# Kernel optimization log

Hardware: AMD Instinct MI355X
Metric: run time of the kernel (lower is better)

## Reference

```python
import jax, jax.numpy as jnp
import numpy as np

B, L = 8, 2048
AMP, ANG = 48, 16
H = 4
AQK, GQK = 12, 6   # amp/ang qk head dims
AV, GV = 12, 6     # amp/ang v head dims
LOOKBACK = 100


def setup_inputs() -> dict:
    key = jax.random.key(0)
    ks = jax.random.split(key, 16)
    def w(k, i, o):
        # kaiming-uniform-ish scale; stored [in, out] so forward is x @ W
        bound = 1.0 / np.sqrt(i)
        return jax.random.uniform(k, (i, o), jnp.float32, -bound, bound)
    return dict(
        x_ang=jax.random.normal(ks[0], (B, L, 2 * ANG), jnp.float32),
        x_amp=jax.random.normal(ks[1], (B, L, AMP), jnp.float32),
        Wq_amp=w(ks[2], AMP, H * AQK),
        Wk_amp=w(ks[3], AMP, H * AQK),
        Wv_amp=w(ks[4], AMP, H * AV),
        Wq_ang_r=w(ks[5], ANG, H * GQK),
        Wq_ang_i=w(ks[6], ANG, H * GQK),
        Wk_ang_r=w(ks[7], ANG, H * GQK),
        Wk_ang_i=w(ks[8], ANG, H * GQK),
        Wv_ang_r=w(ks[9], ANG, H * GV),
        Wv_ang_i=w(ks[10], ANG, H * GV),
        Wout_amp=w(ks[11], H * AV, AMP),
        bout_amp=jax.random.uniform(ks[12], (AMP,), jnp.float32, -0.1, 0.1),
        Wout_ang_r=w(ks[13], H * GV, ANG),
        Wout_ang_i=w(ks[14], H * GV, ANG),
    )


def _clin(xr, xi, Wr, Wi):
    # complex linear: (xr + i xi) @ (Wr + i Wi)
    return xr @ Wr - xi @ Wi, xr @ Wi + xi @ Wr


def reference(x_ang, x_amp, Wq_amp, Wk_amp, Wv_amp,
              Wq_ang_r, Wq_ang_i, Wk_ang_r, Wk_ang_i,
              Wv_ang_r, Wv_ang_i, Wout_amp, bout_amp,
              Wout_ang_r, Wout_ang_i):
    Bb, Ll, CA = x_ang.shape
    ang_r, ang_i = jnp.split(x_ang, 2, axis=-1)

    def heads(x, hd):  # [B,L,H*hd] -> [B,H,L,hd]
        return x.reshape(Bb, Ll, H, hd).transpose(0, 2, 1, 3)

    q_amp = heads(x_amp @ Wq_amp, AQK)
    k_amp = heads(x_amp @ Wk_amp, AQK)
    qar, qai = _clin(ang_r, ang_i, Wq_ang_r, Wq_ang_i)
    kar, kai = _clin(ang_r, ang_i, Wk_ang_r, Wk_ang_i)
    q = jnp.concatenate([heads(qar, GQK), heads(qai, GQK), q_amp], axis=-1)  # [B,H,L,24]
    k = jnp.concatenate([heads(kar, GQK), heads(kai, GQK), k_amp], axis=-1)

    v_amp = heads(x_amp @ Wv_amp, AV)
    var, vai = _clin(ang_r, ang_i, Wv_ang_r, Wv_ang_i)
    v = jnp.concatenate([heads(var, GV), heads(vai, GV), v_amp], axis=-1)  # [B,H,L,24]

    scale = 1.0 / jnp.sqrt(jnp.asarray(q.shape[-1], q.dtype))
    scores = jnp.einsum('bhqd,bhkd->bhqk', q, k) * scale
    idx = jnp.arange(Ll)
    valid = (idx[None, :] <= idx[:, None]) & (idx[None, :] >= idx[:, None] - (LOOKBACK - 1))
    mask = jnp.where(valid, jnp.asarray(0.0, scores.dtype), jnp.finfo(scores.dtype).min)
    attn = jax.nn.softmax(scores + mask, axis=-1)
    out = jnp.einsum('bhqk,bhkd->bhqd', attn, v)  # [B,H,L,24]

    o_ang_r, o_ang_i, o_amp = jnp.split(out, [GV, 2 * GV], axis=-1)

    def merge(x):  # [B,H,L,hd] -> [B,L,H*hd]
        return x.transpose(0, 2, 1, 3).reshape(Bb, Ll, -1)

    out_amp = merge(o_amp) @ Wout_amp + bout_amp
    out_ang_r, out_ang_i = _clin(merge(o_ang_r), merge(o_ang_i), Wout_ang_r, Wout_ang_i)
    return (out_ang_r, out_ang_i, out_amp)
```

## Files before the change

kernel.cpp:

```cpp
#include <hip/hip_runtime.h>
#include <hip/hip_bf16.h>

constexpr int B = 8;
constexpr int L = 2048;
constexpr int ANG = 16;
constexpr int AMP = 48;
constexpr int H = 4;
constexpr int AQK = 12, GQK = 6;
constexpr int AV = 12, GV = 6;
constexpr int HD = 2 * GQK + AQK;
constexpr int LOOKBACK = 100;
constexpr int NTOK = B * L;

constexpr int TQ     = 64;
constexpr int GROUPS = 4;
constexpr int MAXK   = TQ + LOOKBACK - 1;
constexpr int NT     = L / TQ;

struct StageT {
    float xam[MAXK][49];
    float xan[MAXK][33];
};
struct TileT {
    float4 Ks[MAXK][8];
    float4 Vs[MAXK][8];
    float4 Qs[TQ][6];
};
union SharedU { StageT stage; TileT t; };

__global__ __launch_bounds__(256) void fused_qkv_attn_kernel(
    const float* __restrict__ x_ang, const float* __restrict__ x_amp,
    const float* __restrict__ Wq_amp, const float* __restrict__ Wk_amp,
    const float* __restrict__ Wv_amp,
    const float* __restrict__ Wq_ang_r, const float* __restrict__ Wq_ang_i,
    const float* __restrict__ Wk_ang_r, const float* __restrict__ Wk_ang_i,
    const float* __restrict__ Wv_ang_r, const float* __restrict__ Wv_ang_i,
    float* __restrict__ att)
{
    __shared__ SharedU u;
    __shared__ float  Pm[GROUPS][TQ];
    __shared__ float  Ps[GROUPS][TQ];
    __shared__ float4 Po[GROUPS][TQ][6];

    const int tid = threadIdx.x;
    const int bh  = blockIdx.x / NT;
    const int qt  = blockIdx.x % NT;
    const int b   = bh / H, h = bh % H;
    const int q0  = qt * TQ;
    int kmin = q0 - (LOOKBACK - 1); if (kmin < 0) kmin = 0;
    const int nrows = (q0 + TQ - 1) - kmin + 1;
    const int qoff  = q0 - kmin;

    {
        const float4* xm4 = (const float4*)(x_amp + ((size_t)b * L + kmin) * AMP);
        const float4* xg4 = (const float4*)(x_ang + ((size_t)b * L + kmin) * (2 * ANG));
        int namp = nrows * 12;
        int ntot = namp + nrows * 8;
        for (int c = tid; c < ntot; c += 256) {
            if (c < namp) {
                int r = c / 12, i = c % 12;
                float4 t = xm4[c];
                float* p = &u.stage.xam[r][4 * i];
                p[0] = t.x; p[1] = t.y; p[2] = t.z; p[3] = t.w;
            } else {
                int c2 = c - namp;
                int r = c2 / 8, i = c2 % 8;
                float4 t = xg4[c2];
                float* p = &u.stage.xan[r][4 * i];
                p[0] = t.x; p[1] = t.y; p[2] = t.z; p[3] = t.w;
            }
        }
    }
    __syncthreads();

    float4 kout[6], vout[6], qout[6];
    const bool kvact = (tid < nrows);
    const bool qact  = (tid >= 192);
    const int  qrow  = tid - 192;

    #pragma unroll
    for (int s = 0; s < 6; ++s) {
        if (kvact) {
            int r = tid;
            if (s >= 3) {
                int col4 = h * AQK + (s - 3) * 4;
                const float* Wk = Wk_amp + col4;
                const float* Wv = Wv_amp + col4;
                float4 ka = {0,0,0,0}, va = {0,0,0,0};
                #pragma unroll
                for (int i = 0; i < AMP; ++i) {
                    float x = u.stage.xam[r][i];
                    float4 wk = *(const float4*)(Wk + i * 48);
                    float4 wv = *(const float4*)(Wv + i * 48);
                    ka.x += x * wk.x; ka.y += x * wk.y; ka.z += x * wk.z; ka.w += x * wk.w;
                    va.x += x * wv.x; va.y += x * wv.y; va.z += x * wv.z; va.w += x * wv.w;
                }
                kout[s] = ka; vout[s] = va;
            } else {
                float kk[4], vv[4];
                #pragma unroll
                for (int c = 0; c < 4; ++c) {
                    int d = 4 * s + c;
                    bool re = (d < GQK);
                    int dd = re ? d : d - GQK;
                    int col = h * GQK + dd;
                    const float* WkA = re ? Wk_ang_r : Wk_ang_i;
                    const float* WkB = re ? Wk_ang_i : Wk_ang_r;
                    const float* WvA = re ? Wv_ang_r : Wv_ang_i;
                    const float* WvB = re ? Wv_ang_i : Wv_ang_r;
                    float sgn = re ? -1.f : 1.f;
                    float ak = 0, bk = 0, aw = 0, bw = 0;
                    #pragma unroll
                    for (int i = 0; i < ANG; ++i) {
                        float xr = u.stage.xan[r][i];
                        float xi = u.stage.xan[r][16 + i];
                        ak += xr * WkA[i * 24 + col];  bk += xi * WkB[i * 24 + col];
                        aw += xr * WvA[i * 24 + col];  bw += xi * WvB[i * 24 + col];
                    }
                    kk[c] = ak + sgn * bk;  vv[c] = aw + sgn * bw;
                }
                kout[s] = make_float4(kk[0], kk[1], kk[2], kk[3]);
                vout[s] = make_float4(vv[0], vv[1], vv[2], vv[3]);
            }
        }
        if (qact) {
            int r = qoff + qrow;
            if (s >= 3) {
                int col4 = h * AQK + (s - 3) * 4;
                const float* Wq = Wq_amp + col4;
                float4 qa = {0,0,0,0};
                #pragma unroll
                for (int i = 0; i < AMP; ++i) {
                    float x = u.stage.xam[r][i];
                    float4 wq = *(const float4*)(Wq + i * 48);
                    qa.x += x * wq.x; qa.y += x * wq.y; qa.z += x * wq.z; qa.w += x * wq.w;
                }
                qout[s] = qa;
            } else {
                float qq[4];
                #pragma unroll
                for (int c = 0; c < 4; ++c) {
                    int d = 4 * s + c;
                    bool re = (d < GQK);
                    int dd = re ? d : d - GQK;
                    int col = h * GQK + dd;
                    const float* WA = re ? Wq_ang_r : Wq_ang_i;
                    const float* WB = re ? Wq_ang_i : Wq_ang_r;
                    float sgn = re ? -1.f : 1.f;
                    float aa = 0, bb = 0;
                    #pragma unroll
                    for (int i = 0; i < ANG; ++i) {
                        float xr = u.stage.xan[r][i];
                        float xi = u.stage.xan[r][16 + i];
                        aa += xr * WA[i * 24 + col];  bb += xi * WB[i * 24 + col];
                    }
                    qq[c] = aa + sgn * bb;
                }
                qout[s] = make_float4(qq[0], qq[1], qq[2], qq[3]);
            }
        }
    }
    __syncthreads();

    if (kvact) {
        int r = tid, rx = r & 7;
        #pragma unroll
        for (int s = 0; s < 6; ++s) {
            u.t.Ks[r][s ^ rx] = kout[s];
            u.t.Vs[r][s ^ rx] = vout[s];
        }
    }
    if (qact) {
        #pragma unroll
        for (int s = 0; s < 6; ++s) u.t.Qs[qrow][s] = qout[s];
    }
    __syncthreads();

    const int qlocal = tid & (TQ - 1);
    const int group  = tid >> 6;
    const int qi = q0 + qlocal;

    float4 qr4[6];
    #pragma unroll
    for (int s = 0; s < 6; ++s) qr4[s] = u.t.Qs[qlocal][s];

    const float scale = 0.2041241452319315f;
    float m = -3.0e38f, ss = 0.f;
    float4 o4[6];
    #pragma unroll
    for (int s = 0; s < 6; ++s) { o4[s].x = 0.f; o4[s].y = 0.f; o4[s].z = 0.f; o4[s].w = 0.f; }

    int j0 = qi - (LOOKBACK - 1); if (j0 < 0) j0 = 0;
    for (int j = j0 + group; j <= qi; j += GROUPS) {
        int r  = j - kmin;
        int rx = r & 7;
        float sc = 0.f;
        #pragma unroll
        for (int s = 0; s < 6; ++s) {
            float4 kk = u.t.Ks[r][s ^ rx];
            sc += qr4[s].x * kk.x + qr4[s].y * kk.y + qr4[s].z * kk.z + qr4[s].w * kk.w;
        }
        sc *= scale;
        float mn   = fmaxf(m, sc);
        float corr = __expf(m - mn);
        float p    = __expf(sc - mn);
        ss = ss * corr + p;
        #pragma unroll
        for (int s = 0; s < 6; ++s) {
            float4 vv = u.t.Vs[r][s ^ rx];
            o4[s].x = o4[s].x * corr + p * vv.x;
            o4[s].y = o4[s].y * corr + p * vv.y;
            o4[s].z = o4[s].z * corr + p * vv.z;
            o4[s].w = o4[s].w * corr + p * vv.w;
        }
        m = mn;
    }

    Pm[group][qlocal] = m;
    Ps[group][qlocal] = ss;
    #pragma unroll
    for (int s = 0; s < 6; ++s) Po[group][qlocal][s] = o4[s];
    __syncthreads();

    {
        int qq    = tid & 63;
        int chunk = tid >> 6;
        float m0 = Pm[0][qq], m1 = Pm[1][qq], m2 = Pm[2][qq], m3 = Pm[3][qq];
        float mm = fmaxf(fmaxf(m0, m1), fmaxf(m2, m3));
        float c0 = __expf(m0 - mm), c1 = __expf(m1 - mm);
        float c2 = __expf(m2 - mm), c3 = __expf(m3 - mm);
        float denom = Ps[0][qq] * c0 + Ps[1][qq] * c1 + Ps[2][qq] * c2 + Ps[3][qq] * c3;
        float inv = 1.f / denom;

        float4* op4 = (float4*)att + (size_t)(b * L + q0 + qq) * 6 * H / H * H;
        op4 = (float4*)att + ((size_t)(b * L + q0 + qq) * H + h) * 0;
        float4* dst = (float4*)att + (size_t)(b * L + q0 + qq) * 24 + h * 6;

        int s = chunk;
        {
            float4 a0 = Po[0][qq][s], a1 = Po[1][qq][s], a2 = Po[2][qq][s], a3 = Po[3][qq][s];
            float4 acc;
            acc.x = (a0.x * c0 + a1.x * c1 + a2.x * c2 + a3.x * c3) * inv;
            acc.y = (a0.y * c0 + a1.y * c1 + a2.y * c2 + a3.y * c3) * inv;
            acc.z = (a0.z * c0 + a1.z * c1 + a2.z * c2 + a3.z * c3) * inv;
            acc.w = (a0.w * c0 + a1.w * c1 + a2.w * c2 + a3.w * c3) * inv;
            dst[s] = acc;
        }
        if (chunk < 2) {
            s = chunk + 4;
            float4 a0 = Po[0][qq][s], a1 = Po[1][qq][s], a2 = Po[2][qq][s], a3 = Po[3][qq][s];
            float4 acc;
            acc.x = (a0.x * c0 + a1.x * c1 + a2.x * c2 + a3.x * c3) * inv;
            acc.y = (a0.y * c0 + a1.y * c1 + a2.y * c2 + a3.y * c3) * inv;
            acc.z = (a0.z * c0 + a1.z * c1 + a2.z * c2 + a3.z * c3) * inv;
            acc.w = (a0.w * c0 + a1.w * c1 + a2.w * c2 + a3.w * c3) * inv;
            dst[s] = acc;
        }
    }
}

constexpr int PAMP_BLOCKS = (NTOK * 48) / 256;
constexpr int PANG_BLOCKS = (NTOK * 16) / 256;

__global__ __launch_bounds__(256) void proj3_kernel(
    const float* __restrict__ att,
    const float* __restrict__ Wout_amp, const float* __restrict__ bout_amp,
    const float* __restrict__ Wout_ang_r, const float* __restrict__ Wout_ang_i,
    float* __restrict__ out)
{
    constexpr size_t ANG_OUT = (size_t)NTOK * ANG;
    int bid = blockIdx.x;

    if (bid < PAMP_BLOCKS) {
        int g   = bid * 256 + threadIdx.x;
        int col = g % 48;
        int tok = g / 48;
        const float4* at4 = (const float4*)att + (size_t)tok * 24;

        float a[48];
        #pragma unroll
        for (int h = 0; h < H; h++) {
            #pragma unroll
            for (int i = 0; i < 3; i++) {
                float4 t = at4[h * 6 + 3 + i];
                a[h*12 + 4*i+0] = t.x; a[h*12 + 4*i+1] = t.y;
                a[h*12 + 4*i+2] = t.z; a[h*12 + 4*i+3] = t.w;
            }
        }
        float acc = bout_amp[col];
        #pragma unroll
        for (int i = 0; i < 48; i++)
            acc += a[i] * Wout_amp[i * AMP + col];
        out[2 * ANG_OUT + (size_t)tok * AMP + col] = acc;
    } else {
        int g   = (bid - PAMP_BLOCKS) * 256 + threadIdx.x;
        int col = g % 16;
        int tok = g / 16;
        const float4* at4 = (const float4*)att + (size_t)tok * 24;

        float ar[24], ai[24];
        #pragma unroll
        for (int h = 0; h < H; h++) {
            float4 t0 = at4[h*6+0], t1 = at4[h*6+1], t2 = at4[h*6+2];
            ar[h*6+0] = t0.x; ar[h*6+1] = t0.y; ar[h*6+2] = t0.z; ar[h*6+3] = t0.w;
            ar[h*6+4] = t1.x; ar[h*6+5] = t1.y;
            ai[h*6+0] = t1.z; ai[h*6+1] = t1.w;
            ai[h*6+2] = t2.x; ai[h*6+3] = t2.y; ai[h*6+4] = t2.z; ai[h*6+5] = t2.w;
        }
        float accr = 0.f, acci = 0.f;
        #pragma unroll
        for (int i = 0; i < 24; i++) {
            float wr = Wout_ang_r[i * ANG + col], wi = Wout_ang_i[i * ANG + col];
            accr += ar[i] * wr - ai[i] * wi;
            acci += ar[i] * wi + ai[i] * wr;
        }
        out[(size_t)tok * ANG + col]           = accr;
        out[ANG_OUT + (size_t)tok * ANG + col] = acci;
    }
}

extern "C" void kernel_launch(void* const* d_in, const int* in_sizes, int n_in,
                              void* d_out, int out_size, void* d_ws, size_t ws_size,
                              hipStream_t stream)
{
    const float* x_ang      = (const float*)d_in[0];
    const float* x_amp      = (const float*)d_in[1];
    const float* Wq_amp     = (const float*)d_in[2];
    const float* Wk_amp     = (const float*)d_in[3];
    const float* Wv_amp     = (const float*)d_in[4];
    const float* Wq_ang_r   = (const float*)d_in[5];
    const float* Wq_ang_i   = (const float*)d_in[6];
    const float* Wk_ang_r   = (const float*)d_in[7];
    const float* Wk_ang_i   = (const float*)d_in[8];
    const float* Wv_ang_r   = (const float*)d_in[9];
    const float* Wv_ang_i   = (const float*)d_in[10];
    const float* Wout_amp   = (const float*)d_in[11];
    const float* bout_amp   = (const float*)d_in[12];
    const float* Wout_ang_r = (const float*)d_in[13];
    const float* Wout_ang_i = (const float*)d_in[14];

    float* out = (float*)d_out;
    float* att = (float*)d_ws;

    fused_qkv_attn_kernel<<<B * H * NT, 256, 0, stream>>>(
        x_ang, x_amp, Wq_amp, Wk_amp, Wv_amp,
        Wq_ang_r, Wq_ang_i, Wk_ang_r, Wk_ang_i, Wv_ang_r, Wv_ang_i,
        att);

    proj3_kernel<<<PAMP_BLOCKS + PANG_BLOCKS, 256, 0, stream>>>(
        att, Wout_amp, bout_amp, Wout_ang_r, Wout_ang_i, out);
}
```

Before: 153.2 us.

## Load inputs directly to registers, chunked two-pass softmax, vectorize output projection

The QKV projection no longer stages x rows through shared memory. Each thread now loads its own row into registers and computes all 24 head dims in one pass, which removes a staging phase and a barrier. The online-softmax loop becomes a fixed 25-step unrolled two-pass softmax with masking, so the per-key rescaling is gone. The output projection now computes four columns per thread with float4 weight loads and stores. The trade-off is much higher register pressure from the 48-float input arrays and the 25-entry score array, plus masked wasted work on out-of-window keys.

New measurement: 181.6 us. 18.5% more time.

```diff
diff --git a/kernel.cpp b/kernel.cpp
--- a/kernel.cpp
+++ b/kernel.cpp
@@ -14,21 +14,11 @@
 
 constexpr int TQ     = 64;
 constexpr int GROUPS = 4;
+constexpr int CHUNK  = 25;
 constexpr int MAXK   = TQ + LOOKBACK - 1;
 constexpr int NT     = L / TQ;
 
-struct StageT {
-    float xam[MAXK][49];
-    float xan[MAXK][33];
-};
-struct TileT {
-    float4 Ks[MAXK][8];
-    float4 Vs[MAXK][8];
-    float4 Qs[TQ][6];
-};
-union SharedU { StageT stage; TileT t; };
-
-__global__ __launch_bounds__(256) void fused_qkv_attn_kernel(
+__global__ __launch_bounds__(256) void fused_qkv_attn2_kernel(
     const float* __restrict__ x_ang, const float* __restrict__ x_amp,
     const float* __restrict__ Wq_amp, const float* __restrict__ Wk_amp,
     const float* __restrict__ Wv_amp,
@@ -37,10 +27,10 @@
     const float* __restrict__ Wv_ang_r, const float* __restrict__ Wv_ang_i,
     float* __restrict__ att)
 {
-    __shared__ SharedU u;
-    __shared__ float  Pm[GROUPS][TQ];
-    __shared__ float  Ps[GROUPS][TQ];
-    __shared__ float4 Po[GROUPS][TQ][6];
+    __shared__ float4 Ks[MAXK][8];
+    __shared__ float4 Vs[MAXK][8];
+    __shared__ float4 Qs[TQ][7];
+    __shared__ float4 Po[GROUPS][TQ][7];
 
     const int tid = threadIdx.x;
     const int bh  = blockIdx.x / NT;
@@ -48,221 +38,245 @@
     const int b   = bh / H, h = bh % H;
     const int q0  = qt * TQ;
     int kmin = q0 - (LOOKBACK - 1); if (kmin < 0) kmin = 0;
-    const int nrows = (q0 + TQ - 1) - kmin + 1;
-    const int qoff  = q0 - kmin;
-
-    {
-        const float4* xm4 = (const float4*)(x_amp + ((size_t)b * L + kmin) * AMP);
-        const float4* xg4 = (const float4*)(x_ang + ((size_t)b * L + kmin) * (2 * ANG));
-        int namp = nrows * 12;
-        int ntot = namp + nrows * 8;
-        for (int c = tid; c < ntot; c += 256) {
-            if (c < namp) {
-                int r = c / 12, i = c % 12;
-                float4 t = xm4[c];
-                float* p = &u.stage.xam[r][4 * i];
-                p[0] = t.x; p[1] = t.y; p[2] = t.z; p[3] = t.w;
-            } else {
-                int c2 = c - namp;
-                int r = c2 / 8, i = c2 % 8;
-                float4 t = xg4[c2];
-                float* p = &u.stage.xan[r][4 * i];
-                p[0] = t.x; p[1] = t.y; p[2] = t.z; p[3] = t.w;
-            }
-        }
-    }
-    __syncthreads();
-
-    float4 kout[6], vout[6], qout[6];
+    const int nrows = q0 + TQ - kmin;
+
     const bool kvact = (tid < nrows);
     const bool qact  = (tid >= 192);
     const int  qrow  = tid - 192;
 
-    #pragma unroll
-    for (int s = 0; s < 6; ++s) {
-        if (kvact) {
-            int r = tid;
-            if (s >= 3) {
-                int col4 = h * AQK + (s - 3) * 4;
-                const float* Wk = Wk_amp + col4;
-                const float* Wv = Wv_amp + col4;
-                float4 ka = {0,0,0,0}, va = {0,0,0,0};
-                #pragma unroll
-                for (int i = 0; i < AMP; ++i) {
-                    float x = u.stage.xam[r][i];
-                    float4 wk = *(const float4*)(Wk + i * 48);
-                    float4 wv = *(const float4*)(Wv + i * 48);
-                    ka.x += x * wk.x; ka.y += x * wk.y; ka.z += x * wk.z; ka.w += x * wk.w;
-                    va.x += x * wv.x; va.y += x * wv.y; va.z += x * wv.z; va.w += x * wv.w;
-                }
-                kout[s] = ka; vout[s] = va;
-            } else {
-                float kk[4], vv[4];
-                #pragma unroll
-                for (int c = 0; c < 4; ++c) {
-                    int d = 4 * s + c;
-                    bool re = (d < GQK);
-                    int dd = re ? d : d - GQK;
-                    int col = h * GQK + dd;
-                    const float* WkA = re ? Wk_ang_r : Wk_ang_i;
-                    const float* WkB = re ? Wk_ang_i : Wk_ang_r;
-                    const float* WvA = re ? Wv_ang_r : Wv_ang_i;
-                    const float* WvB = re ? Wv_ang_i : Wv_ang_r;
-                    float sgn = re ? -1.f : 1.f;
-                    float ak = 0, bk = 0, aw = 0, bw = 0;
-                    #pragma unroll
-                    for (int i = 0; i < ANG; ++i) {
-                        float xr = u.stage.xan[r][i];
-                        float xi = u.stage.xan[r][16 + i];
-                        ak += xr * WkA[i * 24 + col];  bk += xi * WkB[i * 24 + col];
-                        aw += xr * WvA[i * 24 + col];  bw += xi * WvB[i * 24 + col];
-                    }
-                    kk[c] = ak + sgn * bk;  vv[c] = aw + sgn * bw;
-                }
-                kout[s] = make_float4(kk[0], kk[1], kk[2], kk[3]);
-                vout[s] = make_float4(vv[0], vv[1], vv[2], vv[3]);
-            }
-        }
-        if (qact) {
-            int r = qoff + qrow;
-            if (s >= 3) {
-                int col4 = h * AQK + (s - 3) * 4;
-                const float* Wq = Wq_amp + col4;
-                float4 qa = {0,0,0,0};
-                #pragma unroll
-                for (int i = 0; i < AMP; ++i) {
-                    float x = u.stage.xam[r][i];
-                    float4 wq = *(const float4*)(Wq + i * 48);
-                    qa.x += x * wq.x; qa.y += x * wq.y; qa.z += x * wq.z; qa.w += x * wq.w;
-                }
-                qout[s] = qa;
-            } else {
-                float qq[4];
-                #pragma unroll
-                for (int c = 0; c < 4; ++c) {
-                    int d = 4 * s + c;
-                    bool re = (d < GQK);
-                    int dd = re ? d : d - GQK;
-                    int col = h * GQK + dd;
-                    const float* WA = re ? Wq_ang_r : Wq_ang_i;
-                    const float* WB = re ? Wq_ang_i : Wq_ang_r;
-                    float sgn = re ? -1.f : 1.f;
-                    float aa = 0, bb = 0;
-                    #pragma unroll
-                    for (int i = 0; i < ANG; ++i) {
-                        float xr = u.stage.xan[r][i];
-                        float xi = u.stage.xan[r][16 + i];
-                        aa += xr * WA[i * 24 + col];  bb += xi * WB[i * 24 + col];
-                    }
-                    qq[c] = aa + sgn * bb;
-                }
-                qout[s] = make_float4(qq[0], qq[1], qq[2], qq[3]);
-            }
-        }
-    }
-    __syncthreads();
+    float4 kpack[6], vpack[6], qpack[6];
+
+    if (kvact) {
+        const int row = kmin + tid;
+        float xm[48], xr[16], xi[16];
+        {
+            const float4* xm4 = (const float4*)(x_amp + ((size_t)b * L + row) * AMP);
+            #pragma unroll
+            for (int i = 0; i < 12; ++i) {
+                float4 t = xm4[i];
+                xm[4*i+0]=t.x; xm[4*i+1]=t.y; xm[4*i+2]=t.z; xm[4*i+3]=t.w;
+            }
+            const float4* xg4 = (const float4*)(x_ang + ((size_t)b * L + row) * (2*ANG));
+            #pragma unroll
+            for (int i = 0; i < 4; ++i) {
+                float4 t = xg4[i];
+                xr[4*i+0]=t.x; xr[4*i+1]=t.y; xr[4*i+2]=t.z; xr[4*i+3]=t.w;
+                float4 u = xg4[4+i];
+                xi[4*i+0]=u.x; xi[4*i+1]=u.y; xi[4*i+2]=u.z; xi[4*i+3]=u.w;
+            }
+        }
+        float ka[12], va[12], kr[6], ki[6], vr[6], vi[6];
+        #pragma unroll
+        for (int c = 0; c < 12; ++c) { ka[c]=0.f; va[c]=0.f; }
+        #pragma unroll
+        for (int c = 0; c < 6; ++c) { kr[c]=0.f; ki[c]=0.f; vr[c]=0.f; vi[c]=0.f; }
+
+        #pragma unroll
+        for (int i = 0; i < AMP; ++i) {
+            const float* wk = Wk_amp + i * 48 + h * AQK;
+            const float* wv = Wv_amp + i * 48 + h * AQK;
+            float x = xm[i];
+            #pragma unroll
+            for (int c = 0; c < 12; ++c) {
+                ka[c] += x * wk[c];
+                va[c] += x * wv[c];
+            }
+        }
+        #pragma unroll
+        for (int i = 0; i < ANG; ++i) {
+            const float* wkr = Wk_ang_r + i * 24 + h * GQK;
+            const float* wki = Wk_ang_i + i * 24 + h * GQK;
+            const float* wvr = Wv_ang_r + i * 24 + h * GQK;
+            const float* wvi = Wv_ang_i + i * 24 + h * GQK;
+            float a = xr[i], bb = xi[i];
+            #pragma unroll
+            for (int c = 0; c < 6; ++c) {
+                kr[c] += a * wkr[c] - bb * wki[c];
+                ki[c] += a * wki[c] + bb * wkr[c];
+                vr[c] += a * wvr[c] - bb * wvi[c];
+                vi[c] += a * wvi[c] + bb * wvr[c];
+            }
+        }
+        kpack[0] = make_float4(kr[0],kr[1],kr[2],kr[3]);
+        kpack[1] = make_float4(kr[4],kr[5],ki[0],ki[1]);
+        kpack[2] = make_float4(ki[2],ki[3],ki[4],ki[5]);
+        kpack[3] = make_float4(ka[0],ka[1],ka[2],ka[3]);
+        kpack[4] = make_float4(ka[4],ka[5],ka[6],ka[7]);
+        kpack[5] = make_float4(ka[8],ka[9],ka[10],ka[11]);
+        vpack[0] = make_float4(vr[0],vr[1],vr[2],vr[3]);
+        vpack[1] = make_float4(vr[4],vr[5],vi[0],vi[1]);
+        vpack[2] = make_float4(vi[2],vi[3],vi[4],vi[5]);
+        vpack[3] = make_float4(va[0],va[1],va[2],va[3]);
+        vpack[4] = make_float4(va[4],va[5],va[6],va[7]);
+        vpack[5] = make_float4(va[8],va[9],va[10],va[11]);
+    }
+    if (qact) {
+        const int row = q0 + qrow;
+        float xm[48], xr[16], xi[16];
+        {
+            const float4* xm4 = (const float4*)(x_amp + ((size_t)b * L + row) * AMP);
+            #pragma unroll
+            for (int i = 0; i < 12; ++i) {
+                float4 t = xm4[i];
+                xm[4*i+0]=t.x; xm[4*i+1]=t.y; xm[4*i+2]=t.z; xm[4*i+3]=t.w;
+            }
+            const float4* xg4 = (const float4*)(x_ang + ((size_t)b * L + row) * (2*ANG));
+            #pragma unroll
+            for (int i = 0; i < 4; ++i) {
+                float4 t = xg4[i];
+                xr[4*i+0]=t.x; xr[4*i+1]=t.y; xr[4*i+2]=t.z; xr[4*i+3]=t.w;
+                float4 u = xg4[4+i];
+                xi[4*i+0]=u.x; xi[4*i+1]=u.y; xi[4*i+2]=u.z; xi[4*i+3]=u.w;
+            }
+        }
+        float qa[12], qrr[6], qii[6];
+        #pragma unroll
+        for (int c = 0; c < 12; ++c) qa[c]=0.f;
+        #pragma unroll
+        for (int c = 0; c < 6; ++c) { qrr[c]=0.f; qii[c]=0.f; }
+
+        #pragma unroll
+        for (int i = 0; i < AMP; ++i) {
+            const float* wq = Wq_amp + i * 48 + h * AQK;
+            float x = xm[i];
+            #pragma unroll
+            for (int c = 0; c < 12; ++c) qa[c] += x * wq[c];
+        }
+        #pragma unroll
+        for (int i = 0; i < ANG; ++i) {
+            const float* wr = Wq_ang_r + i * 24 + h * GQK;
+            const float* wi = Wq_ang_i + i * 24 + h * GQK;
+            float a = xr[i], bb = xi[i];
+            #pragma unroll
+            for (int c = 0; c < 6; ++c) {
+                qrr[c] += a * wr[c] - bb * wi[c];
+                qii[c] += a * wi[c] + bb * wr[c];
+            }
+        }
+        qpack[0] = make_float4(qrr[0],qrr[1],qrr[2],qrr[3]);
+        qpack[1] = make_float4(qrr[4],qrr[5],qii[0],qii[1]);
+        qpack[2] = make_float4(qii[2],qii[3],qii[4],qii[5]);
+        qpack[3] = make_float4(qa[0],qa[1],qa[2],qa[3]);
+        qpack[4] = make_float4(qa[4],qa[5],qa[6],qa[7]);
+        qpack[5] = make_float4(qa[8],qa[9],qa[10],qa[11]);
+    }
 
     if (kvact) {
         int r = tid, rx = r & 7;
         #pragma unroll
         for (int s = 0; s < 6; ++s) {
-            u.t.Ks[r][s ^ rx] = kout[s];
-            u.t.Vs[r][s ^ rx] = vout[s];
-        }
+            Ks[r][s ^ rx] = kpack[s];
+            Vs[r][s ^ rx] = vpack[s];
+        }
+    } else if (tid < MAXK) {
+        float4 z = make_float4(0.f,0.f,0.f,0.f);
+        #pragma unroll
+        for (int s = 0; s < 6; ++s) { Ks[tid][s] = z; Vs[tid][s] = z; }
     }
     if (qact) {
         #pragma unroll
-        for (int s = 0; s < 6; ++s) u.t.Qs[qrow][s] = qout[s];
+        for (int s = 0; s < 6; ++s) Qs[qrow][s] = qpack[s];
     }
     __syncthreads();
 
-    const int qlocal = tid & (TQ - 1);
-    const int group  = tid >> 6;
-    const int qi = q0 + qlocal;
-
-    float4 qr4[6];
-    #pragma unroll
-    for (int s = 0; s < 6; ++s) qr4[s] = u.t.Qs[qlocal][s];
+    const int ql = tid & (TQ - 1);
+    const int g  = tid >> 6;
+    const int qi = q0 + ql;
+
+    float4 q4[6];
+    #pragma unroll
+    for (int s = 0; s < 6; ++s) q4[s] = Qs[ql][s];
 
     const float scale = 0.2041241452319315f;
-    float m = -3.0e38f, ss = 0.f;
-    float4 o4[6];
-    #pragma unroll
-    for (int s = 0; s < 6; ++s) { o4[s].x = 0.f; o4[s].y = 0.f; o4[s].z = 0.f; o4[s].w = 0.f; }
-
     int j0 = qi - (LOOKBACK - 1); if (j0 < 0) j0 = 0;
-    for (int j = j0 + group; j <= qi; j += GROUPS) {
+    const int jstart = j0 + g;
+
+    float sc[CHUNK];
+    #pragma unroll
+    for (int t = 0; t < CHUNK; ++t) {
+        int j  = jstart + t * GROUPS;
         int r  = j - kmin;
         int rx = r & 7;
-        float sc = 0.f;
+        float d = 0.f;
         #pragma unroll
         for (int s = 0; s < 6; ++s) {
-            float4 kk = u.t.Ks[r][s ^ rx];
-            sc += qr4[s].x * kk.x + qr4[s].y * kk.y + qr4[s].z * kk.z + qr4[s].w * kk.w;
-        }
-        sc *= scale;
-        float mn   = fmaxf(m, sc);
-        float corr = __expf(m - mn);
-        float p    = __expf(sc - mn);
-        ss = ss * corr + p;
+            float4 kk = Ks[r][s ^ rx];
+            d += q4[s].x*kk.x + q4[s].y*kk.y + q4[s].z*kk.z + q4[s].w*kk.w;
+        }
+        sc[t] = (j <= qi) ? d * scale : -3.0e38f;
+    }
+    float m = sc[0];
+    #pragma unroll
+    for (int t = 1; t < CHUNK; ++t) m = fmaxf(m, sc[t]);
+    float ssum = 0.f;
+    #pragma unroll
+    for (int t = 0; t < CHUNK; ++t) {
+        float p = __expf(sc[t] - m);
+        p = (sc[t] > -1.0e37f) ? p : 0.f;
+        sc[t] = p;
+        ssum += p;
+    }
+    float4 o[6];
+    #pragma unroll
+    for (int s = 0; s < 6; ++s) o[s] = make_float4(0.f,0.f,0.f,0.f);
+    #pragma unroll
+    for (int t = 0; t < CHUNK; ++t) {
+        float p  = sc[t];
+        int j    = jstart + t * GROUPS;
+        int r    = j - kmin;
+        int rx   = r & 7;
         #pragma unroll
         for (int s = 0; s < 6; ++s) {
-            float4 vv = u.t.Vs[r][s ^ rx];
-            o4[s].x = o4[s].x * corr + p * vv.x;
-            o4[s].y = o4[s].y * corr + p * vv.y;
-            o4[s].z = o4[s].z * corr + p * vv.z;
-            o4[s].w = o4[s].w * corr + p * vv.w;
-        }
-        m = mn;
-    }
-
-    Pm[group][qlocal] = m;
-    Ps[group][qlocal] = ss;
-    #pragma unroll
-    for (int s = 0; s < 6; ++s) Po[group][qlocal][s] = o4[s];
+            float4 vv = Vs[r][s ^ rx];
+            o[s].x += p * vv.x; o[s].y += p * vv.y;
+            o[s].z += p * vv.z; o[s].w += p * vv.w;
+        }
+    }
+
+    #pragma unroll
+    for (int s = 0; s < 6; ++s) Po[g][ql][s] = o[s];
+    Po[g][ql][6] = make_float4(m, ssum, 0.f, 0.f);
     __syncthreads();
 
     {
         int qq    = tid & 63;
         int chunk = tid >> 6;
-        float m0 = Pm[0][qq], m1 = Pm[1][qq], m2 = Pm[2][qq], m3 = Pm[3][qq];
-        float mm = fmaxf(fmaxf(m0, m1), fmaxf(m2, m3));
-        float c0 = __expf(m0 - mm), c1 = __expf(m1 - mm);
-        float c2 = __expf(m2 - mm), c3 = __expf(m3 - mm);
-        float denom = Ps[0][qq] * c0 + Ps[1][qq] * c1 + Ps[2][qq] * c2 + Ps[3][qq] * c3;
-        float inv = 1.f / denom;
-
-        float4* op4 = (float4*)att + (size_t)(b * L + q0 + qq) * 6 * H / H * H;
-        op4 = (float4*)att + ((size_t)(b * L + q0 + qq) * H + h) * 0;
+        float4 ms0 = Po[0][qq][6], ms1 = Po[1][qq][6];
+        float4 ms2 = Po[2][qq][6], ms3 = Po[3][qq][6];
+        float mm = fmaxf(fmaxf(ms0.x, ms1.x), fmaxf(ms2.x, ms3.x));
+        float c0 = __expf(ms0.x - mm), c1 = __expf(ms1.x - mm);
+        float c2 = __expf(ms2.x - mm), c3 = __expf(ms3.x - mm);
+        float inv = 1.f / (ms0.y*c0 + ms1.y*c1 + ms2.y*c2 + ms3.y*c3);
+
         float4* dst = (float4*)att + (size_t)(b * L + q0 + qq) * 24 + h * 6;
 
         int s = chunk;
         {
             float4 a0 = Po[0][qq][s], a1 = Po[1][qq][s], a2 = Po[2][qq][s], a3 = Po[3][qq][s];
             float4 acc;
-            acc.x = (a0.x * c0 + a1.x * c1 + a2.x * c2 + a3.x * c3) * inv;
-            acc.y = (a0.y * c0 + a1.y * c1 + a2.y * c2 + a3.y * c3) * inv;
-            acc.z = (a0.z * c0 + a1.z * c1 + a2.z * c2 + a3.z * c3) * inv;
-            acc.w = (a0.w * c0 + a1.w * c1 + a2.w * c2 + a3.w * c3) * inv;
+            acc.x = (a0.x*c0 + a1.x*c1 + a2.x*c2 + a3.x*c3) * inv;
+            acc.y = (a0.y*c0 + a1.y*c1 + a2.y*c2 + a3.y*c3) * inv;
+            acc.z = (a0.z*c0 + a1.z*c1 + a2.z*c2 + a3.z*c3) * inv;
+            acc.w = (a0.w*c0 + a1.w*c1 + a2.w*c2 + a3.w*c3) * inv;
             dst[s] = acc;
         }
         if (chunk < 2) {
             s = chunk + 4;
             float4 a0 = Po[0][qq][s], a1 = Po[1][qq][s], a2 = Po[2][qq][s], a3 = Po[3][qq][s];
             float4 acc;
-            acc.x = (a0.x * c0 + a1.x * c1 + a2.x * c2 + a3.x * c3) * inv;
-            acc.y = (a0.y * c0 + a1.y * c1 + a2.y * c2 + a3.y * c3) * inv;
-            acc.z = (a0.z * c0 + a1.z * c1 + a2.z * c2 + a3.z * c3) * inv;
-            acc.w = (a0.w * c0 + a1.w * c1 + a2.w * c2 + a3.w * c3) * inv;
+            acc.x = (a0.x*c0 + a1.x*c1 + a2.x*c2 + a3.x*c3) * inv;
+            acc.y = (a0.y*c0 + a1.y*c1 + a2.y*c2 + a3.y*c3) * inv;
+            acc.z = (a0.z*c0 + a1.z*c1 + a2.z*c2 + a3.z*c3) * inv;
+            acc.w = (a0.w*c0 + a1.w*c1 + a2.w*c2 + a3.w*c3) * inv;
             dst[s] = acc;
         }
     }
 }
 
-constexpr int PAMP_BLOCKS = (NTOK * 48) / 256;
-constexpr int PANG_BLOCKS = (NTOK * 16) / 256;
-
-__global__ __launch_bounds__(256) void proj3_kernel(
+constexpr int PJ_AMP_BLOCKS = (NTOK * 12) / 256;
+constexpr int PJ_ANG_BLOCKS = (NTOK * 4) / 256;
+
+__global__ __launch_bounds__(256) void proj4_kernel(
     const float* __restrict__ att,
     const float* __restrict__ Wout_amp, const float* __restrict__ bout_amp,
     const float* __restrict__ Wout_ang_r, const float* __restrict__ Wout_ang_i,
@@ -271,51 +285,58 @@
     constexpr size_t ANG_OUT = (size_t)NTOK * ANG;
     int bid = blockIdx.x;
 
-    if (bid < PAMP_BLOCKS) {
-        int g   = bid * 256 + threadIdx.x;
-        int col = g % 48;
-        int tok = g / 48;
+    if (bid < PJ_AMP_BLOCKS) {
+        int gidx = bid * 256 + threadIdx.x;
+        int c4   = (gidx % 12) * 4;
+        int tok  = gidx / 12;
         const float4* at4 = (const float4*)att + (size_t)tok * 24;
 
         float a[48];
         #pragma unroll
-        for (int h = 0; h < H; h++) {
-            #pragma unroll
-            for (int i = 0; i < 3; i++) {
+        for (int h = 0; h < H; ++h) {
+            #pragma unroll
+            for (int i = 0; i < 3; ++i) {
                 float4 t = at4[h * 6 + 3 + i];
-                a[h*12 + 4*i+0] = t.x; a[h*12 + 4*i+1] = t.y;
-                a[h*12 + 4*i+2] = t.z; a[h*12 + 4*i+3] = t.w;
-            }
-        }
-        float acc = bout_amp[col];
-        #pragma unroll
-        for (int i = 0; i < 48; i++)
-            acc += a[i] * Wout_amp[i * AMP + col];
-        out[2 * ANG_OUT + (size_t)tok * AMP + col] = acc;
+                a[h*12 + 4*i+0]=t.x; a[h*12 + 4*i+1]=t.y;
+                a[h*12 + 4*i+2]=t.z; a[h*12 + 4*i+3]=t.w;
+            }
+        }
+        float4 acc = *(const float4*)(bout_amp + c4);
+        #pragma unroll
+        for (int i = 0; i < 48; ++i) {
+            float4 w = *(const float4*)(Wout_amp + i * 48 + c4);
+            acc.x += a[i]*w.x; acc.y += a[i]*w.y; acc.z += a[i]*w.z; acc.w += a[i]*w.w;
+        }
+        *(float4*)(out + 2*ANG_OUT + (size_t)tok * 48 + c4) = acc;
     } else {
-        int g   = (bid - PAMP_BLOCKS) * 256 + threadIdx.x;
-        int col = g % 16;
-        int tok = g / 16;
+        int gidx = (bid - PJ_AMP_BLOCKS) * 256 + threadIdx.x;
+        int c4   = (gidx % 4) * 4;
+        int tok  = gidx / 4;
         const float4* at4 = (const float4*)att + (size_t)tok * 24;
 
         float ar[24], ai[24];
         #pragma unroll
-        for (int h = 0; h < H; h++) {
+        for (int h = 0; h < H; ++h) {
             float4 t0 = at4[h*6+0], t1 = at4[h*6+1], t2 = at4[h*6+2];
-            ar[h*6+0] = t0.x; ar[h*6+1] = t0.y; ar[h*6+2] = t0.z; ar[h*6+3] = t0.w;
-            ar[h*6+4] = t1.x; ar[h*6+5] = t1.y;
-            ai[h*6+0] = t1.z; ai[h*6+1] = t1.w;
-            ai[h*6+2] = t2.x; ai[h*6+3] = t2.y; ai[h*6+4] = t2.z; ai[h*6+5] = t2.w;
-        }
-        float accr = 0.f, acci = 0.f;
-        #pragma unroll
-        for (int i = 0; i < 24; i++) {
-            float wr = Wout_ang_r[i * ANG + col], wi = Wout_ang_i[i * ANG + col];
-            accr += ar[i] * wr - ai[i] * wi;
-            acci += ar[i] * wi + ai[i] * wr;
-        }
-        out[(size_t)tok * ANG + col]           = accr;
-        out[ANG_OUT + (size_t)tok * ANG + col] = acci;
+            ar[h*6+0]=t0.x; ar[h*6+1]=t0.y; ar[h*6+2]=t0.z; ar[h*6+3]=t0.w;
+            ar[h*6+4]=t1.x; ar[h*6+5]=t1.y;
+            ai[h*6+0]=t1.z; ai[h*6+1]=t1.w;
+            ai[h*6+2]=t2.x; ai[h*6+3]=t2.y; ai[h*6+4]=t2.z; ai[h*6+5]=t2.w;
+        }
+        float4 accr = make_float4(0.f,0.f,0.f,0.f);
+        float4 acci = make_float4(0.f,0.f,0.f,0.f);
+        #pragma unroll
+        for (int i = 0; i < 24; ++i) {
+            float4 wr = *(const float4*)(Wout_ang_r + i * 16 + c4);
+            float4 wi = *(const float4*)(Wout_ang_i + i * 16 + c4);
+            float r = ar[i], im = ai[i];
+            accr.x += r*wr.x - im*wi.x;  accr.y += r*wr.y - im*wi.y;
+            accr.z += r*wr.z - im*wi.z;  accr.w += r*wr.w - im*wi.w;
+            acci.x += r*wi.x + im*wr.x;  acci.y += r*wi.y + im*wr.y;
+            acci.z += r*wi.z + im*wr.z;  acci.w += r*wi.w + im*wr.w;
+        }
+        *(float4*)(out + (size_t)tok * 16 + c4)           = accr;
+        *(float4*)(out + ANG_OUT + (size_t)tok * 16 + c4) = acci;
     }
 }
 
@@ -342,11 +363,11 @@
     float* out = (float*)d_out;
     float* att = (float*)d_ws;
 
-    fused_qkv_attn_kernel<<<B * H * NT, 256, 0, stream>>>(
+    fused_qkv_attn2_kernel<<<B * H * NT, 256, 0, stream>>>(
         x_ang, x_amp, Wq_amp, Wk_amp, Wv_amp,
         Wq_ang_r, Wq_ang_i, Wk_ang_r, Wk_ang_i, Wv_ang_r, Wv_ang_i,
         att);
 
-    proj3_kernel<<<PAMP_BLOCKS + PANG_BLOCKS, 256, 0, stream>>>(
+    proj4_kernel<<<PJ_AMP_BLOCKS + PJ_ANG_BLOCKS, 256, 0, stream>>>(
         att, Wout_amp, bout_amp, Wout_ang_r, Wout_ang_i, out);
 }
```
